# Optimization experiments

Measured on AMD Instinct MI355X. Metric: run time of the kernel, lower is better.

The kernel has to match this reference:

```python
import jax, jax.numpy as jnp
import numpy as np

ALPHA = 0.1
MAX_ITER = 35
TOL = 0.01
STEP = ALPHA / 2.0  # step_size = alpha/2 as in TV2DFunction.forward


def _prox_tv1d(step, y):
    """Exact 1D TV prox via taut-string lower/upper hulls (faithful port of _prox_tv1d)."""
    n = y.shape[0]
    width = n + 1
    dt = y.dtype
    cs = jnp.cumsum(y)
    y_low = jnp.concatenate([jnp.zeros(1, dt), cs - step]).at[width - 1].add(step)
    y_up = jnp.concatenate([jnp.zeros(1, dt), cs + step]).at[width - 1].add(-step)

    inf = jnp.asarray(jnp.inf, dt)
    il = jnp.zeros(width, jnp.int32)   # index_low
    iu = jnp.zeros(width, jnp.int32)   # index_up
    idx = jnp.zeros(width, jnp.int32)  # breakpoint indices
    sl = jnp.zeros(width, dt).at[0].set(inf)    # slope_low
    su = jnp.zeros(width, dt).at[0].set(-inf)   # slope_up
    z = jnp.zeros(width, dt)
    zero = jnp.int32(0)

    def fdiv(num, a, b):
        # a > b always holds on the taken branch; maximum() only guards the
        # unselected jnp.where branch against NaN/Inf.
        return num / jnp.maximum(a - b, 1).astype(dt)

    def body(i, st):
        il, sl, iu, su, idx, z, s_l, c_l, s_u, c_u, c = st
        c_l = c_l + 1
        c_u = c_u + 1
        il = il.at[c_l].set(i)
        iu = iu.at[c_u].set(i)
        sl = sl.at[c_l].set(y_low[i] - y_low[i - 1])

        def w1_cond(t):
            il_, sl_, c_l_ = t
            return (c_l_ > s_l + 1) & (sl_[jnp.maximum(s_l, c_l_ - 1)] <= sl_[c_l_])

        def w1_body(t):
            il_, sl_, c_l_ = t
            c_l_ = c_l_ - 1
            il_ = il_.at[c_l_].set(i)
            ns = jnp.where(c_l_ > s_l + 1,
                           fdiv(y_low[i] - y_low[il_[c_l_ - 1]], i, il_[c_l_ - 1]),
                           fdiv(y_low[i] - z[c], i, idx[c]))
            return il_, sl_.at[c_l_].set(ns), c_l_

        il, sl, c_l = jax.lax.while_loop(w1_cond, w1_body, (il, sl, c_l))

        su = su.at[c_u].set(y_up[i] - y_up[i - 1])

        def w2_cond(t):
            iu_, su_, c_u_ = t
            return (c_u_ > s_u + 1) & (su_[jnp.maximum(s_u, c_u_ - 1)] >= su_[c_u_])

        def w2_body(t):
            iu_, su_, c_u_ = t
            c_u_ = c_u_ - 1
            iu_ = iu_.at[c_u_].set(i)
            ns = jnp.where(c_u_ > s_u + 1,
                           fdiv(y_up[i] - y_up[iu_[c_u_ - 1]], i, iu_[c_u_ - 1]),
                           fdiv(y_up[i] - z[c], i, idx[c]))
            return iu_, su_.at[c_u_].set(ns), c_u_

        iu, su, c_u = jax.lax.while_loop(w2_cond, w2_body, (iu, su, c_u))

        def w3_cond(t):
            idx_, z_, sl_, il_, s_u_, c_ = t
            return (c_l == s_l + 1) & (c_u > s_u_ + 1) & (sl_[c_l] >= su[s_u_ + 1])

        def w3_body(t):
            idx_, z_, sl_, il_, s_u_, c_ = t
            c_ = c_ + 1
            s_u_ = s_u_ + 1
            k = iu[s_u_]
            idx_ = idx_.at[c_].set(k)
            z_ = z_.at[c_].set(y_up[k])
            il_ = il_.at[s_l].set(k)
            sl_ = sl_.at[c_l].set(fdiv(y_low[i] - y_up[k], i, k))
            return idx_, z_, sl_, il_, s_u_, c_

        idx, z, sl, il, s_u, c = jax.lax.while_loop(w3_cond, w3_body, (idx, z, sl, il, s_u, c))

        def w4_cond(t):
            idx_, z_, su_, iu_, s_l_, c_ = t
            return (c_u == s_u + 1) & (c_l > s_l_ + 1) & (su_[c_u] <= sl[s_l_ + 1])

        def w4_body(t):
            idx_, z_, su_, iu_, s_l_, c_ = t
            c_ = c_ + 1
            s_l_ = s_l_ + 1
            k = il[s_l_]
            idx_ = idx_.at[c_].set(k)
            z_ = z_.at[c_].set(y_low[k])
            iu_ = iu_.at[s_u].set(k)
            su_ = su_.at[c_u].set(fdiv(y_up[i] - y_low[k], i, k))
            return idx_, z_, su_, iu_, s_l_, c_

        idx, z, su, iu, s_l, c = jax.lax.while_loop(w4_cond, w4_body, (idx, z, su, iu, s_l, c))

        return il, sl, iu, su, idx, z, s_l, c_l, s_u, c_u, c

    st = (il, sl, iu, su, idx, z, zero, zero, zero, zero, zero)
    il, sl, iu, su, idx, z, s_l, c_l, s_u, c_u, c = jax.lax.fori_loop(1, width, body, st)

    # tail: append remaining lower-hull points to the breakpoint list
    m = c_l - s_l
    offs = jnp.arange(width)
    valid = (offs >= 1) & (offs <= m)
    src = il[jnp.clip(s_l + offs, 0, width - 1)]
    tgt = jnp.where(valid, c + offs, width)  # 'width' is out of bounds -> dropped
    idx = idx.at[tgt].set(src, mode='drop')
    z = z.at[tgt].set(y_low[src], mode='drop')
    c = c + m

    # piecewise-constant output: slope of taut string on each segment
    a = (z - jnp.roll(z, 1)) / jnp.maximum(idx - jnp.roll(idx, 1), 1).astype(dt)
    knots = jnp.where(offs <= c, idx, n + 1)  # sorted; idx[c] == n
    seg = jnp.searchsorted(knots, jnp.arange(n), side='right')  # segment id in [1, c]
    return a[seg]


def _prox_cols(step, A):
    return jax.vmap(lambda col: _prox_tv1d(step, col), in_axes=1, out_axes=1)(A)


def _prox_rows(step, A):
    return jax.vmap(lambda row: _prox_tv1d(step, row))(A)


def _prox_tv2d(x, step, max_iter, tol):
    """Douglas-Rachford splitting for 2D TV prox (Barbero & Sra 2014)."""
    def cond(carry):
        it, x_, p, q, acc = carry
        return (it < max_iter) & (acc >= tol)

    def body(carry):
        it, x_, p, q, _ = carry
        y = _prox_cols(step, x_ + p)
        p = p + x_ - y
        x2 = _prox_rows(step, y + q)
        q = q + y - x2
        acc = jnp.max(jnp.abs(y - x2))
        return it + 1, x2, p, q, acc

    z0 = jnp.zeros_like(x)
    init = (jnp.int32(0), x, z0, z0, jnp.asarray(jnp.inf, x.dtype))
    return jax.lax.while_loop(cond, body, init)[1]


def setup_inputs() -> dict:
    key = jax.random.key(0)
    X = jax.random.normal(key, (256, 256), dtype=jnp.float32)
    return {"X": X}


def reference(X):
    return _prox_tv2d(X, STEP, MAX_ITER, TOL)
```

## Files before the change

### kernel.cpp

```cpp
#include <hip/hip_runtime.h>

#define N 256
#define NB 256
#define NT 64
#define LAM 0.05f
#define TWOLAM (2.0f * LAM)
#define FOURLAM (4.0f * LAM)
#define MAXIT 35
#define TOL 0.01f
#define SLOTSTRIDE 2

__device__ __forceinline__ float rlane(float v, int lane) {
    return __int_as_float(__builtin_amdgcn_readlane(__float_as_int(v), lane));
}

__device__ __forceinline__ void gstore(float* p, float v) {
    __hip_atomic_store(p, v, __ATOMIC_RELAXED, __HIP_MEMORY_SCOPE_AGENT);
}

__device__ __forceinline__ void gload_col(const float* mat, int c, int lane, float& a,
                                          float& b, float& d, float& e) {
    const float* p0 = mat + (size_t)lane * N + c;
    const float* p1 = p0 + 64 * N;
    const float* p2 = p0 + 128 * N;
    const float* p3 = p0 + 192 * N;
    asm volatile("global_load_dword %0, %4, off sc0 sc1\n\t"
                 "global_load_dword %1, %5, off sc0 sc1\n\t"
                 "global_load_dword %2, %6, off sc0 sc1\n\t"
                 "global_load_dword %3, %7, off sc0 sc1\n\t"
                 "s_waitcnt vmcnt(0)"
                 : "=&v"(a), "=&v"(b), "=&v"(d), "=&v"(e)
                 : "v"(p0), "v"(p1), "v"(p2), "v"(p3)
                 : "memory");
}

struct Dist { float r0, r1, r2, r3; };

__device__ __forceinline__ float dfetch(const Dist& d, int k) {
    const int lane = k & 63;
    const int sel = k >> 6;
    float a = rlane(d.r0, lane);
    float b = rlane(d.r1, lane);
    float c = rlane(d.r2, lane);
    float e = rlane(d.r3, lane);
    float ab = (sel & 1) ? b : a;
    float ce = (sel & 1) ? e : c;
    return (sel & 2) ? ce : ab;
}

__device__ __forceinline__ void flushseg(Dist& o, int lo, int hi, float val, int lane) {
    const unsigned len = (unsigned)(hi - lo);
    const int base = lane - lo;
    o.r0 = ((unsigned)(base      ) <= len) ? val : o.r0;
    o.r1 = ((unsigned)(base + 64 ) <= len) ? val : o.r1;
    o.r2 = ((unsigned)(base + 128) <= len) ? val : o.r2;
    o.r3 = ((unsigned)(base + 192) <= len) ? val : o.r3;
}

__device__ __forceinline__ unsigned long long sel4(unsigned long long a, unsigned long long b,
                                                   unsigned long long c, unsigned long long d, int r) {
    unsigned long long ab = (r & 1) ? b : a;
    unsigned long long cd = (r & 1) ? d : c;
    return (r & 2) ? cd : ab;
}

__device__ __forceinline__ unsigned wredmax(unsigned x) {
    unsigned t;
    t = (unsigned)__builtin_amdgcn_update_dpp(0, (int)x, 0x111, 0xf, 0xf, true); x = x > t ? x : t;
    t = (unsigned)__builtin_amdgcn_update_dpp(0, (int)x, 0x112, 0xf, 0xf, true); x = x > t ? x : t;
    t = (unsigned)__builtin_amdgcn_update_dpp(0, (int)x, 0x114, 0xf, 0xf, true); x = x > t ? x : t;
    t = (unsigned)__builtin_amdgcn_update_dpp(0, (int)x, 0x118, 0xf, 0xf, true); x = x > t ? x : t;
    t = (unsigned)__builtin_amdgcn_update_dpp(0, (int)x, 0x142, 0xf, 0xf, true); x = x > t ? x : t;
    t = (unsigned)__builtin_amdgcn_update_dpp(0, (int)x, 0x143, 0xf, 0xf, true); x = x > t ? x : t;
    return (unsigned)__builtin_amdgcn_readlane((int)x, 63);
}

__device__ void tv1d_scan(const Dist& v, Dist& o, const int lane)
{
    const float lam = LAM, mlam = -LAM, twolam = TWOLAM;

    Dist vnx;
    {
        float a0 = __shfl_down(v.r0, 1), a1 = __shfl_down(v.r1, 1);
        float a2 = __shfl_down(v.r2, 1), a3 = __shfl_down(v.r3, 1);
        const bool hi = (lane == 63);
        vnx.r0 = hi ? rlane(v.r1, 0) : a0;
        vnx.r1 = hi ? rlane(v.r2, 0) : a1;
        vnx.r2 = hi ? rlane(v.r3, 0) : a2;
        vnx.r3 = hi ? v.r3 : a3;
    }
    Dist d;
    d.r0 = vnx.r0 - v.r0;  d.r1 = vnx.r1 - v.r1;
    d.r2 = vnx.r2 - v.r2;  d.r3 = vnx.r3 - v.r3;
    const unsigned lambits = __float_as_uint(lam);
    Dist sl;
    sl.r0 = __uint_as_float((__float_as_uint(d.r0) & 0x80000000u) | lambits);
    sl.r1 = __uint_as_float((__float_as_uint(d.r1) & 0x80000000u) | lambits);
    sl.r2 = __uint_as_float((__float_as_uint(d.r2) & 0x80000000u) | lambits);
    sl.r3 = __uint_as_float((__float_as_uint(d.r3) & 0x80000000u) | lambits);
    Dist slp;
    {
        float b0 = __shfl_up(sl.r0, 1), b1 = __shfl_up(sl.r1, 1);
        float b2 = __shfl_up(sl.r2, 1), b3 = __shfl_up(sl.r3, 1);
        const bool lo = (lane == 0);
        slp.r0 = lo ? 0.0f : b0;
        slp.r1 = lo ? rlane(sl.r0, 63) : b1;
        slp.r2 = lo ? rlane(sl.r1, 63) : b2;
        slp.r3 = lo ? rlane(sl.r2, 63) : b3;
    }
    Dist e, g;
    {
        float t0 = v.r0 - slp.r0, t1 = v.r1 - slp.r1, t2 = v.r2 - slp.r2, t3 = v.r3 - slp.r3;
        e.r0 = t0 + sl.r0;  e.r1 = t1 + sl.r1;  e.r2 = t2 + sl.r2;  e.r3 = t3 + sl.r3;
        g.r0 = t0 - lam;    g.r1 = t1 - lam;    g.r2 = t2 - lam;    g.r3 = t3 - lam;
    }
    const unsigned long long S0 = __ballot(d.r0 < 0.0f);
    const unsigned long long S1 = __ballot(d.r1 < 0.0f);
    const unsigned long long S2 = __ballot(d.r2 < 0.0f);
    const unsigned long long S3 = __ballot(d.r3 < 0.0f);
    const unsigned long long B20 = __ballot(fabsf(d.r0) > TWOLAM);
    const unsigned long long B21 = __ballot(fabsf(d.r1) > TWOLAM);
    const unsigned long long B22 = __ballot(fabsf(d.r2) > TWOLAM);
    const unsigned long long B23 = __ballot(fabsf(d.r3) > TWOLAM);
    const unsigned long long B40 = __ballot(fabsf(d.r0) > FOURLAM);
    const unsigned long long B41 = __ballot(fabsf(d.r1) > FOURLAM);
    const unsigned long long B42 = __ballot(fabsf(d.r2) > FOURLAM);
    const unsigned long long B43 = __ballot(fabsf(d.r3) > FOURLAM);
    const unsigned long long Sp0 = (S0 << 1);
    const unsigned long long Sp1 = (S1 << 1) | (S0 >> 63);
    const unsigned long long Sp2 = (S2 << 1) | (S1 >> 63);
    const unsigned long long Sp3 = (S3 << 1) | (S2 >> 63);
    const unsigned long long NF0 = ~(B40 | (B20 & ~(S0 ^ Sp0)));
    const unsigned long long NF1 = ~(B41 | (B21 & ~(S1 ^ Sp1)));
    const unsigned long long NF2 = ~(B42 | (B22 & ~(S2 ^ Sp2)));
    const unsigned long long NF3 = ~((B43 | (B23 & ~(S3 ^ Sp3))) & 0x7FFFFFFFFFFFFFFFull);
    const unsigned long long FNn0 = (S0 & B20) | (~S0 & B40);
    const unsigned long long FNn1 = (S1 & B21) | (~S1 & B41);
    const unsigned long long FNn2 = (S2 & B22) | (~S2 & B42);
    const unsigned long long FNn3 = (S3 & B23) | (~S3 & B43);
    const unsigned long long FNp0 = (~S0 & B20) | (S0 & B40);
    const unsigned long long FNp1 = (~S1 & B21) | (S1 & B41);
    const unsigned long long FNp2 = (~S2 & B22) | (S2 & B42);
    const unsigned long long FNp3 = (~S3 & B23) | (S3 & B43);
    const int initFF = (int)(B40 & 1ull);

    auto firstnf = [&](int jmin) -> int {
        const int w = jmin >> 6;
        unsigned long long m = sel4(NF0, NF1, NF2, NF3, w) >> (jmin & 63);
        if (m) return jmin + (int)__builtin_ctzll(m);
        unsigned long long m1 = (w < 1) ? NF1 : 0ull;
        unsigned long long m2 = (w < 2) ? NF2 : 0ull;
        if (m1) return 64 + (int)__builtin_ctzll(m1);
        if (m2) return 128 + (int)__builtin_ctzll(m2);
        return 192 + (int)__builtin_ctzll(NF3);
    };

    auto trigbit = [&](int kk, int neg) -> int {
        const int w = kk >> 6;
        const unsigned long long m = neg ? sel4(FNn0, FNn1, FNn2, FNn3, w)
                                         : sel4(FNp0, FNp1, FNp2, FNp3, w);
        return (int)((m >> (kk & 63)) & 1ull);
    };

    int k = 0, k0 = 0, km = 0, kp = 0;
    float umin = lam, umax = mlam;
    const float v0 = rlane(v.r0, 0);
    float vmin = v0 - lam, vmax = v0 + lam;
    float flen = 1.0f;
    float rnext = 0.5f;
    float vn1 = rlane(vnx.r0, 0);

    auto fastfwd = [&]() {
        const int K1 = firstnf(k + 1);
        const int sneg = (int)((sel4(S0, S1, S2, S3, k >> 6) >> (k & 63)) & 1ull);
        flushseg(o, k, k, sneg ? vmin : vmax, lane);
        if (K1 > k + 1) {
            const int lo = k + 1;
            const unsigned len = (unsigned)(K1 - 1 - lo);
            const int base = lane - lo;
            o.r0 = ((unsigned)(base      ) <= len) ? e.r0 : o.r0;
            o.r1 = ((unsigned)(base + 64 ) <= len) ? e.r1 : o.r1;
            o.r2 = ((unsigned)(base + 128) <= len) ? e.r2 : o.r2;
            o.r3 = ((unsigned)(base + 192) <= len) ? e.r3 : o.r3;
        }
        k = K1; k0 = K1; km = K1; kp = K1;
        vmin = dfetch(g, K1);
        vmax = vmin + twolam;
        umin = lam; umax = mlam;
        flen = 1.0f; rnext = 0.5f;
        vn1 = dfetch(vnx, K1);
    };

    auto do_step = [&]() {
        const float un = umin + vn1 - vmin;
        const float ux = umax + vn1 - vmax;
        const bool neg = un < mlam;
        const bool pos = ux > lam;
        const int wn = (k + 1) >> 6, bn = (k + 1) & 63;
        const int tn = (int)((sel4(FNn0, FNn1, FNn2, FNn3, wn) >> bn) & 1ull);
        const int tp = (int)((sel4(FNp0, FNp1, FNp2, FNp3, wn) >> bn) & 1ull);
        if (__builtin_expect((int)(neg | pos), 1)) {
            const float fval = neg ? vmin : vmax;
            const int   fhi  = neg ? km : kp;
            flushseg(o, k0, fhi, fval, lane);
            const int k0n = fhi + 1;
            float vstar;
            int trig;
            if (__builtin_expect((int)(k0n <= k), 0)) {
                vstar = dfetch(v, k0n);
                trig = trigbit(k0n, (int)neg);
            } else {
                vstar = vn1;
                trig = neg ? tn : tp;
            }
            k = k0n; k0 = k0n; km = k0n; kp = k0n;
            vmin = neg ? vstar : vstar - twolam;
            vmax = vmin + twolam;
            umin = lam; umax = mlam;
            flen = 1.0f; rnext = 0.5f;
            if (k < N - 1 && trig) {
                fastfwd();
            } else {
                vn1 = dfetch(vnx, k);
            }
        } else {
            k++;
            const float r = rnext;
            flen += 1.0f;
            const bool cmin = (un >= lam);
            const bool cmax = (ux <= mlam);
            vmin = cmin ? fmaf(un - lam, r, vmin) : vmin;
            km   = cmin ? k : km;
            umin = cmin ? lam : un;
            vmax = cmax ? fmaf(ux + lam, r, vmax) : vmax;
            kp   = cmax ? k : kp;
            umax = cmax ? mlam : ux;
            vn1 = dfetch(vnx, k);
            rnext = __builtin_amdgcn_rcpf(flen + 1.0f);
        }
    };

    if (initFF) fastfwd();

    for (;;) {
        while (k < N - 1) {
            do_step();
            if (k >= N - 1) break;
            do_step();
        }
        for (;;) {
            if (umin < 0.0f) {
                flushseg(o, k0, km, vmin, lane);
                k0 = km + 1;
                if (k0 > N - 1) return;
                km = k = k0;
                vmin = dfetch(v, k0);
                umin = lam;
                umax = vmin + lam - vmax;
                flen = 1.0f;
            } else if (umax > 0.0f) {
                flushseg(o, k0, kp, vmax, lane);
                k0 = kp + 1;
                if (k0 > N - 1) return;
                kp = k = k0;
                vmax = dfetch(v, k0);
                umax = mlam;
                umin = vmax - lam - vmin;
                flen = 1.0f;
            } else {
                vmin += umin / flen;
                flushseg(o, k0, k, vmin, lane);
                return;
            }
            if (k != N - 1) break;
        }
        rnext = 0.5f;
        vn1 = dfetch(vnx, k);
    }
}

template <bool WANT>
__device__ __forceinline__ unsigned wavebar(unsigned long long* slots, unsigned seq,
                                            unsigned payload, int line, int lane)
{
    __builtin_amdgcn_s_waitcnt(0);
    __hip_atomic_store(&slots[line * SLOTSTRIDE],
                       ((unsigned long long)payload << 32) | (unsigned long long)seq,
                       __ATOMIC_RELAXED, __HIP_MEMORY_SCOPE_AGENT);
    auto ld = [&](int i) {
        return __hip_atomic_load(&slots[i * SLOTSTRIDE],
                                 __ATOMIC_RELAXED, __HIP_MEMORY_SCOPE_AGENT);
    };
    unsigned long long f0 = ld(lane), f1 = ld(lane + 64),
                       f2 = ld(lane + 128), f3 = ld(lane + 192);
    for (;;) {
        unsigned long long g0 = ld(lane), g1 = ld(lane + 64),
                           g2 = ld(lane + 128), g3 = ld(lane + 192);
        const bool ok = ((unsigned)f0 >= seq) & ((unsigned)f1 >= seq) &
                        ((unsigned)f2 >= seq) & ((unsigned)f3 >= seq);
        if (__all((int)ok)) break;
        f0 = g0; f1 = g1; f2 = g2; f3 = g3;
    }
    unsigned ga = 0u;
    if (WANT) {
        unsigned a = (unsigned)(f0 >> 32), b = (unsigned)(f1 >> 32);
        unsigned c = (unsigned)(f2 >> 32), d = (unsigned)(f3 >> 32);
        a = a > b ? a : b;  c = c > d ? c : d;  a = a > c ? a : c;
        ga = wredmax(a);
    }
    return ga;
}

__global__ __launch_bounds__(NT) void tv2d_coop(const float* __restrict__ X,
                                                float* __restrict__ xw,
                                                float* __restrict__ yt,
                                                unsigned long long* __restrict__ slots)
{
    const int lane = threadIdx.x;
    const int b = blockIdx.x;

    Dist p = {0.f, 0.f, 0.f, 0.f};
    Dist q = {0.f, 0.f, 0.f, 0.f};
    unsigned accprev = 0u;

    for (int it = 0; it < MAXIT; ++it) {
        const float* xs = (it == 0) ? X : xw;
        Dist v, o;
        gload_col(xs, b, lane, v.r0, v.r1, v.r2, v.r3);
        v.r0 += p.r0;  v.r1 += p.r1;  v.r2 += p.r2;  v.r3 += p.r3;
        tv1d_scan(v, o, lane);
        p.r0 = v.r0 - o.r0;  p.r1 = v.r1 - o.r1;
        p.r2 = v.r2 - o.r2;  p.r3 = v.r3 - o.r3;
        float* yr = yt + b * N;
        gstore(yr + lane,       o.r0);
        gstore(yr + lane + 64,  o.r1);
        gstore(yr + lane + 128, o.r2);
        gstore(yr + lane + 192, o.r3);
        wavebar<false>(slots, 2u * (unsigned)it + 1u, accprev, b, lane);

        Dist yv, w, o2;
        gload_col(yt, b, lane, yv.r0, yv.r1, yv.r2, yv.r3);
        w.r0 = yv.r0 + q.r0;
        w.r1 = yv.r1 + q.r1;
        w.r2 = yv.r2 + q.r2;
        w.r3 = yv.r3 + q.r3;
        tv1d_scan(w, o2, lane);
        float d0 = yv.r0 - o2.r0;
        float d1 = yv.r1 - o2.r1;
        float d2 = yv.r2 - o2.r2;
        float d3 = yv.r3 - o2.r3;
        q.r0 = w.r0 - o2.r0;  q.r1 = w.r1 - o2.r1;
        q.r2 = w.r2 - o2.r2;  q.r3 = w.r3 - o2.r3;
        float* xr = xw + b * N;
        gstore(xr + lane,       o2.r0);
        gstore(xr + lane + 64,  o2.r1);
        gstore(xr + lane + 128, o2.r2);
        gstore(xr + lane + 192, o2.r3);

        float am = fmaxf(fmaxf(fabsf(d0), fabsf(d1)), fmaxf(fabsf(d2), fabsf(d3)));
        const unsigned amu = wredmax(__float_as_uint(am));

        if (it == MAXIT - 1) break;

        const unsigned ga = wavebar<true>(slots, 2u * (unsigned)it + 2u, amu, b, lane);
        if (__uint_as_float(ga) < TOL) break;
        accprev = amu;
    }
}

extern "C" void kernel_launch(void* const* d_in, const int* in_sizes, int n_in,
                              void* d_out, int out_size, void* d_ws, size_t ws_size,
                              hipStream_t stream) {
    const float* X = (const float*)d_in[0];
    float* xw = (float*)d_out;
    float* yt = (float*)d_ws;
    unsigned long long* slots = (unsigned long long*)((char*)d_ws + (size_t)N * N * sizeof(float));
    (void)hipMemsetAsync((void*)slots, 0, N * SLOTSTRIDE * sizeof(unsigned long long), stream);
    void* args[] = { (void*)&X, (void*)&xw, (void*)&yt, (void*)&slots };
    (void)hipLaunchCooperativeKernel((void*)tv2d_coop, dim3(NB), dim3(NT), args, 0, stream);
}
```

Before: 271.1 us.

## Replace global barriers with per-element sequence-tagged data flags and double buffering

Adds a fused kernel that packs each float with an iteration sequence number into 64-bit words. Each block polls only the column it needs instead of waiting at a grid-wide barrier. Row and column buffers and the convergence values are double-buffered, and the convergence check is deferred so it overlaps the next column prox. The cost is four times more workspace traffic from 64-bit stores and a large memset, plus a spin budget that could silently read stale data if it expires.

```diff
diff --git a/kernel.cpp b/kernel.cpp
--- a/kernel.cpp
+++ b/kernel.cpp
@@ -9,12 +9,21 @@
 #define MAXIT 35
 #define TOL 0.01f
 #define SLOTSTRIDE 2
+#define POLLBUDGET (1 << 17)
+
+typedef unsigned long long u64;
 
 __device__ __forceinline__ float rlane(float v, int lane) {
     return __int_as_float(__builtin_amdgcn_readlane(__float_as_int(v), lane));
 }
 
 __device__ __forceinline__ void gstore(float* p, float v) {
+    __hip_atomic_store(p, v, __ATOMIC_RELAXED, __HIP_MEMORY_SCOPE_AGENT);
+}
+__device__ __forceinline__ u64 ald(const u64* p) {
+    return __hip_atomic_load(p, __ATOMIC_RELAXED, __HIP_MEMORY_SCOPE_AGENT);
+}
+__device__ __forceinline__ void ast(u64* p, u64 v) {
     __hip_atomic_store(p, v, __ATOMIC_RELAXED, __HIP_MEMORY_SCOPE_AGENT);
 }
 
@@ -57,10 +66,9 @@
     o.r3 = ((unsigned)(base + 192) <= len) ? val : o.r3;
 }
 
-__device__ __forceinline__ unsigned long long sel4(unsigned long long a, unsigned long long b,
-                                                   unsigned long long c, unsigned long long d, int r) {
-    unsigned long long ab = (r & 1) ? b : a;
-    unsigned long long cd = (r & 1) ? d : c;
+__device__ __forceinline__ u64 sel4(u64 a, u64 b, u64 c, u64 d, int r) {
+    u64 ab = (r & 1) ? b : a;
+    u64 cd = (r & 1) ? d : c;
     return (r & 2) ? cd : ab;
 }
 
@@ -73,6 +81,36 @@
     t = (unsigned)__builtin_amdgcn_update_dpp(0, (int)x, 0x142, 0xf, 0xf, true); x = x > t ? x : t;
     t = (unsigned)__builtin_amdgcn_update_dpp(0, (int)x, 0x143, 0xf, 0xf, true); x = x > t ? x : t;
     return (unsigned)__builtin_amdgcn_readlane((int)x, 63);
+}
+
+
+__device__ __forceinline__ void pollcol(const u64* m, int c, unsigned seq, int lane, Dist& v) {
+    const u64* p0 = m + (size_t)lane * N + c;
+    const u64* p1 = p0 + 64 * N;
+    const u64* p2 = p0 + 128 * N;
+    const u64* p3 = p0 + 192 * N;
+    u64 f0 = ald(p0), f1 = ald(p1), f2 = ald(p2), f3 = ald(p3);
+    int spin = 0;
+    for (;;) {
+        u64 g0 = ald(p0), g1 = ald(p1), g2 = ald(p2), g3 = ald(p3);
+        const bool ok = ((unsigned)f0 >= seq) & ((unsigned)f1 >= seq) &
+                        ((unsigned)f2 >= seq) & ((unsigned)f3 >= seq);
+        if (__all((int)ok)) break;
+        if (__builtin_expect(++spin > POLLBUDGET, 0)) break;
+        f0 = g0; f1 = g1; f2 = g2; f3 = g3;
+    }
+    v.r0 = __uint_as_float((unsigned)(f0 >> 32));
+    v.r1 = __uint_as_float((unsigned)(f1 >> 32));
+    v.r2 = __uint_as_float((unsigned)(f2 >> 32));
+    v.r3 = __uint_as_float((unsigned)(f3 >> 32));
+}
+
+__device__ __forceinline__ void storerow(u64* m, int row, unsigned seq, const Dist& o, int lane) {
+    u64* r = m + (size_t)row * N;
+    ast(r + lane,       ((u64)__float_as_uint(o.r0) << 32) | (u64)seq);
+    ast(r + lane + 64,  ((u64)__float_as_uint(o.r1) << 32) | (u64)seq);
+    ast(r + lane + 128, ((u64)__float_as_uint(o.r2) << 32) | (u64)seq);
+    ast(r + lane + 192, ((u64)__float_as_uint(o.r3) << 32) | (u64)seq);
 }
 
 __device__ void tv1d_scan(const Dist& v, Dist& o, const int lane)
@@ -114,42 +152,42 @@
         e.r0 = t0 + sl.r0;  e.r1 = t1 + sl.r1;  e.r2 = t2 + sl.r2;  e.r3 = t3 + sl.r3;
         g.r0 = t0 - lam;    g.r1 = t1 - lam;    g.r2 = t2 - lam;    g.r3 = t3 - lam;
     }
-    const unsigned long long S0 = __ballot(d.r0 < 0.0f);
-    const unsigned long long S1 = __ballot(d.r1 < 0.0f);
-    const unsigned long long S2 = __ballot(d.r2 < 0.0f);
-    const unsigned long long S3 = __ballot(d.r3 < 0.0f);
-    const unsigned long long B20 = __ballot(fabsf(d.r0) > TWOLAM);
-    const unsigned long long B21 = __ballot(fabsf(d.r1) > TWOLAM);
-    const unsigned long long B22 = __ballot(fabsf(d.r2) > TWOLAM);
-    const unsigned long long B23 = __ballot(fabsf(d.r3) > TWOLAM);
-    const unsigned long long B40 = __ballot(fabsf(d.r0) > FOURLAM);
-    const unsigned long long B41 = __ballot(fabsf(d.r1) > FOURLAM);
-    const unsigned long long B42 = __ballot(fabsf(d.r2) > FOURLAM);
-    const unsigned long long B43 = __ballot(fabsf(d.r3) > FOURLAM);
-    const unsigned long long Sp0 = (S0 << 1);
-    const unsigned long long Sp1 = (S1 << 1) | (S0 >> 63);
-    const unsigned long long Sp2 = (S2 << 1) | (S1 >> 63);
-    const unsigned long long Sp3 = (S3 << 1) | (S2 >> 63);
-    const unsigned long long NF0 = ~(B40 | (B20 & ~(S0 ^ Sp0)));
-    const unsigned long long NF1 = ~(B41 | (B21 & ~(S1 ^ Sp1)));
-    const unsigned long long NF2 = ~(B42 | (B22 & ~(S2 ^ Sp2)));
-    const unsigned long long NF3 = ~((B43 | (B23 & ~(S3 ^ Sp3))) & 0x7FFFFFFFFFFFFFFFull);
-    const unsigned long long FNn0 = (S0 & B20) | (~S0 & B40);
-    const unsigned long long FNn1 = (S1 & B21) | (~S1 & B41);
-    const unsigned long long FNn2 = (S2 & B22) | (~S2 & B42);
-    const unsigned long long FNn3 = (S3 & B23) | (~S3 & B43);
-    const unsigned long long FNp0 = (~S0 & B20) | (S0 & B40);
-    const unsigned long long FNp1 = (~S1 & B21) | (S1 & B41);
-    const unsigned long long FNp2 = (~S2 & B22) | (S2 & B42);
-    const unsigned long long FNp3 = (~S3 & B23) | (S3 & B43);
+    const u64 S0 = __ballot(d.r0 < 0.0f);
+    const u64 S1 = __ballot(d.r1 < 0.0f);
+    const u64 S2 = __ballot(d.r2 < 0.0f);
+    const u64 S3 = __ballot(d.r3 < 0.0f);
+    const u64 B20 = __ballot(fabsf(d.r0) > TWOLAM);
+    const u64 B21 = __ballot(fabsf(d.r1) > TWOLAM);
+    const u64 B22 = __ballot(fabsf(d.r2) > TWOLAM);
+    const u64 B23 = __ballot(fabsf(d.r3) > TWOLAM);
+    const u64 B40 = __ballot(fabsf(d.r0) > FOURLAM);
+    const u64 B41 = __ballot(fabsf(d.r1) > FOURLAM);
+    const u64 B42 = __ballot(fabsf(d.r2) > FOURLAM);
+    const u64 B43 = __ballot(fabsf(d.r3) > FOURLAM);
+    const u64 Sp0 = (S0 << 1);
+    const u64 Sp1 = (S1 << 1) | (S0 >> 63);
+    const u64 Sp2 = (S2 << 1) | (S1 >> 63);
+    const u64 Sp3 = (S3 << 1) | (S2 >> 63);
+    const u64 NF0 = ~(B40 | (B20 & ~(S0 ^ Sp0)));
+    const u64 NF1 = ~(B41 | (B21 & ~(S1 ^ Sp1)));
+    const u64 NF2 = ~(B42 | (B22 & ~(S2 ^ Sp2)));
+    const u64 NF3 = ~((B43 | (B23 & ~(S3 ^ Sp3))) & 0x7FFFFFFFFFFFFFFFull);
+    const u64 FNn0 = (S0 & B20) | (~S0 & B40);
+    const u64 FNn1 = (S1 & B21) | (~S1 & B41);
+    const u64 FNn2 = (S2 & B22) | (~S2 & B42);
+    const u64 FNn3 = (S3 & B23) | (~S3 & B43);
+    const u64 FNp0 = (~S0 & B20) | (S0 & B40);
+    const u64 FNp1 = (~S1 & B21) | (S1 & B41);
+    const u64 FNp2 = (~S2 & B22) | (S2 & B42);
+    const u64 FNp3 = (~S3 & B23) | (S3 & B43);
     const int initFF = (int)(B40 & 1ull);
 
     auto firstnf = [&](int jmin) -> int {
         const int w = jmin >> 6;
-        unsigned long long m = sel4(NF0, NF1, NF2, NF3, w) >> (jmin & 63);
+        u64 m = sel4(NF0, NF1, NF2, NF3, w) >> (jmin & 63);
         if (m) return jmin + (int)__builtin_ctzll(m);
-        unsigned long long m1 = (w < 1) ? NF1 : 0ull;
-        unsigned long long m2 = (w < 2) ? NF2 : 0ull;
+        u64 m1 = (w < 1) ? NF1 : 0ull;
+        u64 m2 = (w < 2) ? NF2 : 0ull;
         if (m1) return 64 + (int)__builtin_ctzll(m1);
         if (m2) return 128 + (int)__builtin_ctzll(m2);
         return 192 + (int)__builtin_ctzll(NF3);
@@ -157,8 +195,8 @@
 
     auto trigbit = [&](int kk, int neg) -> int {
         const int w = kk >> 6;
-        const unsigned long long m = neg ? sel4(FNn0, FNn1, FNn2, FNn3, w)
-                                         : sel4(FNp0, FNp1, FNp2, FNp3, w);
+        const u64 m = neg ? sel4(FNn0, FNn1, FNn2, FNn3, w)
+                          : sel4(FNp0, FNp1, FNp2, FNp3, w);
         return (int)((m >> (kk & 63)) & 1ull);
     };
 
@@ -279,23 +317,111 @@
     }
 }
 
+__global__ __launch_bounds__(NT) void tv2d_fused(const float* __restrict__ X,
+                                                 float* __restrict__ out,
+                                                 u64* __restrict__ ytg,
+                                                 u64* __restrict__ xwg,
+                                                 u64* __restrict__ accs)
+{
+    const int lane = threadIdx.x;
+    const int b = blockIdx.x;
+
+    Dist p = {0.f, 0.f, 0.f, 0.f};
+    Dist q = {0.f, 0.f, 0.f, 0.f};
+    Dist xout = {0.f, 0.f, 0.f, 0.f};
+
+    for (int it = 0; it < MAXIT; ++it) {
+        Dist v, o;
+        if (it == 0) {
+            gload_col(X, b, lane, v.r0, v.r1, v.r2, v.r3);
+        } else {
+            pollcol(xwg + (size_t)((it - 1) & 1) * (N * N), b, (unsigned)it, lane, v);
+        }
+        v.r0 += p.r0;  v.r1 += p.r1;  v.r2 += p.r2;  v.r3 += p.r3;
+
+        const u64* ab = accs + (size_t)((it - 1) & 1) * (N * 2);
+        const u64 *qa0 = ab + (size_t)lane * 2,        *qa1 = ab + (size_t)(lane + 64) * 2,
+                  *qa2 = ab + (size_t)(lane + 128) * 2, *qa3 = ab + (size_t)(lane + 192) * 2;
+        u64 a0 = 0, a1 = 0, a2 = 0, a3 = 0;
+        if (it >= 1) {
+            asm volatile("global_load_dwordx2 %0, %4, off sc0 sc1\n\t"
+                         "global_load_dwordx2 %1, %5, off sc0 sc1\n\t"
+                         "global_load_dwordx2 %2, %6, off sc0 sc1\n\t"
+                         "global_load_dwordx2 %3, %7, off sc0 sc1"
+                         : "=&v"(a0), "=&v"(a1), "=&v"(a2), "=&v"(a3)
+                         : "v"(qa0), "v"(qa1), "v"(qa2), "v"(qa3)
+                         : "memory");
+        }
+
+        tv1d_scan(v, o, lane);
+        p.r0 = v.r0 - o.r0;  p.r1 = v.r1 - o.r1;
+        p.r2 = v.r2 - o.r2;  p.r3 = v.r3 - o.r3;
+
+        if (it >= 1) {
+            asm volatile("s_waitcnt vmcnt(0)" ::: "memory");
+            const unsigned seq = (unsigned)it;
+            int spin = 0;
+            for (;;) {
+                const bool ok = ((unsigned)a0 >= seq) & ((unsigned)a1 >= seq) &
+                                ((unsigned)a2 >= seq) & ((unsigned)a3 >= seq);
+                if (__all((int)ok)) break;
+                if (__builtin_expect(++spin > POLLBUDGET, 0)) break;
+                a0 = ald(qa0); a1 = ald(qa1); a2 = ald(qa2); a3 = ald(qa3);
+            }
+            unsigned ma = (unsigned)(a0 >> 32), mb = (unsigned)(a1 >> 32);
+            unsigned mc = (unsigned)(a2 >> 32), md = (unsigned)(a3 >> 32);
+            ma = ma > mb ? ma : mb;  mc = mc > md ? mc : md;  ma = ma > mc ? ma : mc;
+            const unsigned gm = wredmax(ma);
+            if (__uint_as_float(gm) < TOL) break;
+        }
+
+        storerow(ytg + (size_t)(it & 1) * (N * N), b, (unsigned)(it + 1), o, lane);
+
+        Dist yv, w, o2;
+        pollcol(ytg + (size_t)(it & 1) * (N * N), b, (unsigned)(it + 1), lane, yv);
+        w.r0 = yv.r0 + q.r0;
+        w.r1 = yv.r1 + q.r1;
+        w.r2 = yv.r2 + q.r2;
+        w.r3 = yv.r3 + q.r3;
+        tv1d_scan(w, o2, lane);
+        q.r0 = w.r0 - o2.r0;  q.r1 = w.r1 - o2.r1;
+        q.r2 = w.r2 - o2.r2;  q.r3 = w.r3 - o2.r3;
+        xout = o2;
+
+        float am = fmaxf(fmaxf(fabsf(yv.r0 - o2.r0), fabsf(yv.r1 - o2.r1)),
+                         fmaxf(fabsf(yv.r2 - o2.r2), fabsf(yv.r3 - o2.r3)));
+        const unsigned amu = wredmax(__float_as_uint(am));
+
+        if (it < MAXIT - 1) {
+            storerow(xwg + (size_t)(it & 1) * (N * N), b, (unsigned)(it + 1), o2, lane);
+            if (lane == 0)
+                ast((u64*)(accs + (size_t)(it & 1) * (N * 2)) + (size_t)b * 2,
+                    ((u64)amu << 32) | (u64)(unsigned)(it + 1));
+        }
+    }
+
+    float* xr = out + (size_t)b * N;
+    xr[lane]       = xout.r0;
+    xr[lane + 64]  = xout.r1;
+    xr[lane + 128] = xout.r2;
+    xr[lane + 192] = xout.r3;
+}
+
 template <bool WANT>
-__device__ __forceinline__ unsigned wavebar(unsigned long long* slots, unsigned seq,
+__device__ __forceinline__ unsigned wavebar(u64* slots, unsigned seq,
                                             unsigned payload, int line, int lane)
 {
     __builtin_amdgcn_s_waitcnt(0);
     __hip_atomic_store(&slots[line * SLOTSTRIDE],
-                       ((unsigned long long)payload << 32) | (unsigned long long)seq,
+                       ((u64)payload << 32) | (u64)seq,
                        __ATOMIC_RELAXED, __HIP_MEMORY_SCOPE_AGENT);
     auto ld = [&](int i) {
         return __hip_atomic_load(&slots[i * SLOTSTRIDE],
                                  __ATOMIC_RELAXED, __HIP_MEMORY_SCOPE_AGENT);
     };
-    unsigned long long f0 = ld(lane), f1 = ld(lane + 64),
-                       f2 = ld(lane + 128), f3 = ld(lane + 192);
+    u64 f0 = ld(lane), f1 = ld(lane + 64), f2 = ld(lane + 128), f3 = ld(lane + 192);
     for (;;) {
-        unsigned long long g0 = ld(lane), g1 = ld(lane + 64),
-                           g2 = ld(lane + 128), g3 = ld(lane + 192);
+        u64 g0 = ld(lane), g1 = ld(lane + 64), g2 = ld(lane + 128), g3 = ld(lane + 192);
         const bool ok = ((unsigned)f0 >= seq) & ((unsigned)f1 >= seq) &
                         ((unsigned)f2 >= seq) & ((unsigned)f3 >= seq);
         if (__all((int)ok)) break;
@@ -314,7 +440,7 @@
 __global__ __launch_bounds__(NT) void tv2d_coop(const float* __restrict__ X,
                                                 float* __restrict__ xw,
                                                 float* __restrict__ yt,
-                                                unsigned long long* __restrict__ slots)
+                                                u64* __restrict__ slots)
 {
     const int lane = threadIdx.x;
     const int b = blockIdx.x;
@@ -373,9 +499,21 @@
                               hipStream_t stream) {
     const float* X = (const float*)d_in[0];
     float* xw = (float*)d_out;
-    float* yt = (float*)d_ws;
-    unsigned long long* slots = (unsigned long long*)((char*)d_ws + (size_t)N * N * sizeof(float));
-    (void)hipMemsetAsync((void*)slots, 0, N * SLOTSTRIDE * sizeof(unsigned long long), stream);
-    void* args[] = { (void*)&X, (void*)&xw, (void*)&yt, (void*)&slots };
-    (void)hipLaunchCooperativeKernel((void*)tv2d_coop, dim3(NB), dim3(NT), args, 0, stream);
-}
+
+    const size_t need = (size_t)4 * N * N * sizeof(u64)
+                      + (size_t)2 * N * 2 * sizeof(u64);
+    if (ws_size >= need) {
+        u64* ytg  = (u64*)d_ws;
+        u64* xwg  = ytg + (size_t)2 * N * N;
+        u64* accs = xwg + (size_t)2 * N * N;
+        (void)hipMemsetAsync(d_ws, 0, need, stream);
+        void* args[] = { (void*)&X, (void*)&xw, (void*)&ytg, (void*)&xwg, (void*)&accs };
+        (void)hipLaunchCooperativeKernel((void*)tv2d_fused, dim3(NB), dim3(NT), args, 0, stream);
+    } else {
+        float* yt = (float*)d_ws;
+        u64* slots = (u64*)((char*)d_ws + (size_t)N * N * sizeof(float));
+        (void)hipMemsetAsync((void*)slots, 0, N * SLOTSTRIDE * sizeof(u64), stream);
+        void* args[] = { (void*)&X, (void*)&xw, (void*)&yt, (void*)&slots };
+        (void)hipLaunchCooperativeKernel((void*)tv2d_coop, dim3(NB), dim3(NT), args, 0, stream);
+    }
+}
```

Result: slower. 288.4 us (+6.4%).
